# Performance work log

Hardware: AMD Instinct MI355X
Metric: run time of the kernel (lower is better)

The kernel has to match this reference:

```python
import jax, jax.numpy as jnp
import numpy as np
import math

HEADS = 4
DK = 64            # dim // heads
TEMP = 1.0
LMAX = 2048        # max segment length (for padded ragged attention)


def setup_inputs() -> dict:
    key = jax.random.key(0)
    ks = jax.random.split(key, 6)
    T, H, B = 1024, 256, 16
    # ragged lengths alternating 2048/1024 -> N = 24576
    lengths = np.tile(np.array([2048, 1024], dtype=np.int64), B // 2)
    N = int(lengths.sum())
    s = 1.0 / math.sqrt(H)
    return {
        "go_mat": jax.random.normal(ks[0], (T, H), jnp.float32),
        "node_h": jax.random.normal(ks[1], (N, H), jnp.float32),
        "Wq": jax.random.normal(ks[2], (H, H), jnp.float32) * s,
        "Wk": jax.random.normal(ks[3], (H, H), jnp.float32) * s,
        "Wv": jax.random.normal(ks[4], (H, H), jnp.float32) * s,
        "Wproj": jax.random.normal(ks[5], (H, H), jnp.float32) * s,
        "num_nodes_per_graph": jnp.asarray(lengths),
    }


def reference(go_mat, node_h, Wq, Wk, Wv, Wproj, num_nodes_per_graph):
    lengths = num_nodes_per_graph
    B = lengths.shape[0]
    N, H = node_h.shape
    T = go_mat.shape[0]

    # segment bookkeeping: graph id and within-graph offset for each node
    cum = jnp.cumsum(lengths)                       # [B]
    starts = cum - lengths                          # [B]
    g = jnp.searchsorted(cum, jnp.arange(N), side="right")  # [N] graph id
    off = jnp.arange(N) - starts[g]                 # [N] position within graph

    # projections (torch Linear: x @ W.T)
    Q = (go_mat @ Wq.T).reshape(T, HEADS, DK).transpose(1, 0, 2)   # [h,T,dk]
    K = node_h @ Wk.T                                              # [N,H]
    V = node_h @ Wv.T

    # scatter packed nodes into padded [B, Lmax, H]
    Kp = jnp.zeros((B, LMAX, H), K.dtype).at[g, off].set(K)
    Vp = jnp.zeros((B, LMAX, H), V.dtype).at[g, off].set(V)
    Kp = Kp.reshape(B, LMAX, HEADS, DK).transpose(0, 2, 1, 3)      # [B,h,L,dk]
    Vp = Vp.reshape(B, LMAX, HEADS, DK).transpose(0, 2, 1, 3)

    scores = jnp.einsum("htd,bhld->bhtl", Q, Kp) / (math.sqrt(DK) * TEMP)
    valid = jnp.arange(LMAX)[None, :] < lengths[:, None]           # [B,L]
    scores = jnp.where(valid[:, None, None, :], scores, jnp.float32(-1e30))
    attn = jax.nn.softmax(scores, axis=-1)                         # [B,h,T,L]

    ctx = jnp.einsum("bhtl,bhld->bhtd", attn, Vp)                  # [B,h,T,dk]
    ctx = ctx.transpose(0, 2, 1, 3).reshape(B, T, H)               # [B,T,H]
    return ctx @ Wproj.T
```

## Files before the change

kernel.cpp:

```cpp
#include <hip/hip_runtime.h>
#include <math.h>

#define HEADS 4
#define DK 64
#define HD 256

typedef __attribute__((ext_vector_type(8))) __bf16 bf16x8;
typedef __attribute__((ext_vector_type(4))) float floatx4;

__device__ __forceinline__ ushort f2bf(float f) {
  union { float f; unsigned u; } x; x.f = f;
  return (ushort)((x.u + 0x7FFF + ((x.u >> 16) & 1)) >> 16);
}

#if __has_builtin(__builtin_amdgcn_exp2f)
#define EXP2(x) __builtin_amdgcn_exp2f(x)
#else
#define EXP2(x) exp2f(x)
#endif

__device__ __forceinline__ unsigned pack_bf2(float lo, float hi) {
  union { float f; unsigned u; } a, b;
  a.f = lo; b.f = hi;
  return __builtin_amdgcn_perm(b.u + 0x8000u, a.u + 0x8000u, 0x07060302u);
}

#define GLDS(g, l) __builtin_amdgcn_global_load_lds(                      \
    (const __attribute__((address_space(1))) unsigned*)(g),               \
    (__attribute__((address_space(3))) unsigned*)(l), 16, 0, 0)

__global__ __launch_bounds__(256) void cvt_fused(
    const float* __restrict__ go, const float* __restrict__ nh,
    const float* __restrict__ w0, const float* __restrict__ w1,
    const float* __restrict__ w2, const float* __restrict__ w3,
    ushort* __restrict__ gobf, ushort* __restrict__ nodebf,
    ushort* __restrict__ wbf, int T, int N) {
  const int idx = blockIdx.x * 256 + threadIdx.x;
  const int row = idx >> 5, gr = idx & 31;
  if (row >= T + N + 4 * 256) return;
  const float* x; ushort* y; int r = row;
  if (row < T) { x = go; y = gobf; }
  else if (row < T + N) { x = nh; y = nodebf; r = row - T; }
  else {
    const int wr = row - T - N, wi = wr >> 8;
    r = wr & 255;
    x = (wi == 0) ? w0 : (wi == 1) ? w1 : (wi == 2) ? w2 : w3;
    y = wbf + (size_t)wi * HD * HD;
  }
  const int chunk = gr >> 3, g = gr & 7;
  const float* src = x + (size_t)r * 256 + gr * 8;
  float4 a = *(const float4*)src;
  float4 bq = *(const float4*)(src + 4);
  ushort* dst = y + (size_t)r * 256 + chunk * 64 + (g ^ (r & 7)) * 8;
  ushort4 o0 = {f2bf(a.x), f2bf(a.y), f2bf(a.z), f2bf(a.w)};
  ushort4 o1 = {f2bf(bq.x), f2bf(bq.y), f2bf(bq.z), f2bf(bq.w)};
  *(ushort4*)dst = o0;
  *(ushort4*)(dst + 4) = o1;
}

__device__ __forceinline__ void gemm_tile(const ushort* __restrict__ A,
                                          const ushort* __restrict__ W,
                                          ushort* __restrict__ C, int m0,
                                          int n0, int mode, int ldc,
                                          ushort* As, ushort* Ws, int lane,
                                          int w, int quad, int l15) {
  const int wm = w & 1, wn = w >> 1;
  floatx4 acc[4][2];
#pragma unroll
  for (int mt = 0; mt < 4; ++mt)
#pragma unroll
    for (int nt = 0; nt < 2; ++nt) acc[mt][nt] = (floatx4){0.f, 0.f, 0.f, 0.f};

  for (int k0 = 0; k0 < 256; k0 += 64) {
    __syncthreads();
#pragma unroll
    for (int t = 0; t < 4; ++t)
      GLDS(A + (size_t)(m0 + w * 32 + t * 8 + (lane >> 3)) * 256 + k0 + (lane & 7) * 8,
           &As[(w * 32 + t * 8) * 64]);
#pragma unroll
    for (int t = 0; t < 2; ++t)
      GLDS(W + (size_t)(n0 + w * 16 + t * 8 + (lane >> 3)) * 256 + k0 + (lane & 7) * 8,
           &Ws[(w * 16 + t * 8) * 64]);
    __syncthreads();

    bf16x8 af[4][2], bfr[2][2];
#pragma unroll
    for (int kk = 0; kk < 2; ++kk) {
      const int pg = ((kk * 4 + quad) ^ (l15 & 7)) * 8;
#pragma unroll
      for (int mt = 0; mt < 4; ++mt)
        af[mt][kk] = *(const bf16x8*)&As[(wm * 64 + mt * 16 + l15) * 64 + pg];
#pragma unroll
      for (int nt = 0; nt < 2; ++nt)
        bfr[nt][kk] = *(const bf16x8*)&Ws[(wn * 32 + nt * 16 + l15) * 64 + pg];
    }
#pragma unroll
    for (int kk = 0; kk < 2; ++kk)
#pragma unroll
      for (int mt = 0; mt < 4; ++mt)
#pragma unroll
        for (int nt = 0; nt < 2; ++nt)
          acc[mt][nt] = __builtin_amdgcn_mfma_f32_16x16x32_bf16(
              af[mt][kk], bfr[nt][kk], acc[mt][nt], 0, 0, 0);
  }

#pragma unroll
  for (int mt = 0; mt < 4; ++mt)
#pragma unroll
    for (int nt = 0; nt < 2; ++nt) {
      const int col = n0 + wn * 32 + nt * 16 + l15;
      if (mode == 2) {
        const int d = col & 63;
        const int g = mt * 2 + (quad >> 1);
        const int node = m0 + wm * 64 + (g ^ (d & 7)) * 8 + (quad & 1) * 4;
        ushort4 o = {f2bf(acc[mt][nt][0]), f2bf(acc[mt][nt][1]),
                     f2bf(acc[mt][nt][2]), f2bf(acc[mt][nt][3])};
        *(ushort4*)&C[(size_t)col * ldc + node] = o;
      } else {
#pragma unroll
        for (int r = 0; r < 4; ++r) {
          const int row = m0 + wm * 64 + mt * 16 + quad * 4 + r;
          if (mode == 3) {
            ((float*)C)[(size_t)row * 256 + col] = acc[mt][nt][r];
          } else {
            int cc = col;
            if (mode == 1)
              cc = (col & ~63) | (((((col >> 3) & 7) ^ (row & 7))) << 3) | (col & 7);
            C[(size_t)row * 256 + cc] = f2bf(acc[mt][nt][r]);
          }
        }
      }
    }
}

__global__ __launch_bounds__(256) void qkv_gemm(const ushort* __restrict__ gobf,
                                                const ushort* __restrict__ nodebf,
                                                const ushort* __restrict__ wbf,
                                                ushort* __restrict__ Qbf,
                                                ushort* __restrict__ Kgb,
                                                ushort* __restrict__ Vtb,
                                                int T, int N) {
  __shared__ __align__(16) ushort As[128 * 64];
  __shared__ __align__(16) ushort Ws[64 * 64];
  const int tid = threadIdx.x, lane = tid & 63, w = tid >> 6;
  const int quad = lane >> 4, l15 = lane & 15;
  const int QX = T >> 7, KB = N >> 7;
  const int NT = QX + 2 * KB;
  const int jx = blockIdx.x % NT;
  const int n0 = (blockIdx.x / NT) * 64;
  if (jx < QX)
    gemm_tile(gobf, wbf, Qbf, jx * 128, n0, 0, 0, As, Ws, lane, w, quad, l15);
  else if (jx < QX + KB)
    gemm_tile(nodebf, wbf + (size_t)HD * HD, Kgb, (jx - QX) * 128, n0, 1, 0,
              As, Ws, lane, w, quad, l15);
  else
    gemm_tile(nodebf, wbf + (size_t)2 * HD * HD, Vtb, (jx - QX - KB) * 128, n0,
              2, N, As, Ws, lane, w, quad, l15);
}

__global__ __launch_bounds__(256, 3) void attn_split(
    const ushort* __restrict__ Qb, const ushort* __restrict__ Kg,
    const ushort* __restrict__ Vt, const int* __restrict__ lens,
    float* __restrict__ Opart, float* __restrict__ Lpart,
    int T, int N, int B) {
  __shared__ __align__(16) ushort Ks[2][64 * 64];
  __shared__ __align__(16) ushort Vs[2][64 * 64];
  __shared__ __align__(16) ushort Ps[4 * 32 * 72];

  const int tid = threadIdx.x, lane = tid & 63, wave = tid >> 6;
  const int quad = lane >> 4, l15 = lane & 15;
  const int QX = T >> 7;
  const int nspl = N >> 10;
  const int grpc = HEADS * nspl;
  const int qx = blockIdx.x / grpc;
  const int rem = blockIdx.x - qx * grpc;
  const int h = rem / nspl;
  const int zid = rem - h * nspl;

  int z = zid, b, start = 0, len = 0, off = -1;
  for (b = 0; b < B; ++b) {
    len = lens[b];
    const int s = (len + 1023) >> 10;
    if (z < s) { off = z << 10; break; }
    z -= s; start += len;
  }
  if (off < 0) return;
  const int kcnt = min(1024, len - off);
  const int kbeg = start + off;

  const int q0 = qx * 128 + wave * 32;
  bf16x8 qb[2][2];
#pragma unroll
  for (int qt = 0; qt < 2; ++qt)
#pragma unroll
    for (int kk = 0; kk < 2; ++kk)
      qb[qt][kk] = *(const bf16x8*)(Qb + (size_t)(q0 + qt * 16 + l15) * 256 +
                                    h * 64 + kk * 32 + quad * 8);

  floatx4 o[2][4];
#pragma unroll
  for (int qt = 0; qt < 2; ++qt)
#pragma unroll
    for (int nt = 0; nt < 4; ++nt) o[qt][nt] = (floatx4){0.f, 0.f, 0.f, 0.f};
  float lsum[2] = {0.f, 0.f};

  const float sc = 0.18033688011112042f;
  ushort* pw = &Ps[wave * 32 * 72];
  const int srow = lane >> 3;
  const int scol = (lane & 7) * 8;

  GLDS(Kg + (size_t)(kbeg + wave * 8 + srow) * 256 + h * 64 + scol,
       &Ks[0][(wave * 8) * 64]);
  GLDS(Kg + (size_t)(kbeg + wave * 8 + 32 + srow) * 256 + h * 64 + scol,
       &Ks[0][(wave * 8 + 32) * 64]);
  GLDS(Vt + (size_t)(h * 64 + wave * 8 + srow) * (size_t)N + kbeg + scol,
       &Vs[0][(wave * 8) * 64]);
  GLDS(Vt + (size_t)(h * 64 + wave * 8 + 32 + srow) * (size_t)N + kbeg + scol,
       &Vs[0][(wave * 8 + 32) * 64]);

  int buf = 0;
  for (int j0 = 0; j0 < kcnt; j0 += 64, buf ^= 1) {
    __syncthreads();
    const int jn = j0 + 64;
    if (jn < kcnt) {
      GLDS(Kg + (size_t)(kbeg + jn + wave * 8 + srow) * 256 + h * 64 + scol,
           &Ks[buf ^ 1][(wave * 8) * 64]);
      GLDS(Kg + (size_t)(kbeg + jn + wave * 8 + 32 + srow) * 256 + h * 64 + scol,
           &Ks[buf ^ 1][(wave * 8 + 32) * 64]);
      GLDS(Vt + (size_t)(h * 64 + wave * 8 + srow) * (size_t)N + kbeg + jn + scol,
           &Vs[buf ^ 1][(wave * 8) * 64]);
      GLDS(Vt + (size_t)(h * 64 + wave * 8 + 32 + srow) * (size_t)N + kbeg + jn + scol,
           &Vs[buf ^ 1][(wave * 8 + 32) * 64]);
    }

    floatx4 st[4][2];
#pragma unroll
    for (int t = 0; t < 4; ++t)
#pragma unroll
      for (int qt = 0; qt < 2; ++qt) st[t][qt] = (floatx4){0.f, 0.f, 0.f, 0.f};
#pragma unroll
    for (int kk = 0; kk < 2; ++kk) {
#pragma unroll
      for (int t = 0; t < 4; ++t) {
        bf16x8 kf = *(const bf16x8*)&Ks[buf][(t * 16 + l15) * 64 +
                                            ((kk * 4 + quad) ^ (l15 & 7)) * 8];
        st[t][0] = __builtin_amdgcn_mfma_f32_16x16x32_bf16(kf, qb[0][kk], st[t][0], 0, 0, 0);
        st[t][1] = __builtin_amdgcn_mfma_f32_16x16x32_bf16(kf, qb[1][kk], st[t][1], 0, 0, 0);
      }
    }

    if (jn <= kcnt) {
#pragma unroll
      for (int t = 0; t < 4; ++t)
#pragma unroll
        for (int qt = 0; qt < 2; ++qt) {
          float p[4];
#pragma unroll
          for (int r = 0; r < 4; ++r) p[r] = EXP2(fmaf(st[t][qt][r], sc, -32.0f));
          lsum[qt] += (p[0] + p[1]) + (p[2] + p[3]);
          uint2 pk = {pack_bf2(p[0], p[1]), pack_bf2(p[2], p[3])};
          *(uint2*)&pw[(qt * 16 + l15) * 72 + t * 16 + quad * 4] = pk;
        }
    } else {
#pragma unroll
      for (int t = 0; t < 4; ++t)
#pragma unroll
        for (int qt = 0; qt < 2; ++qt) {
          float p[4];
#pragma unroll
          for (int r = 0; r < 4; ++r) {
            const bool v = (j0 + t * 16 + quad * 4 + r) < kcnt;
            p[r] = v ? EXP2(fmaf(st[t][qt][r], sc, -32.0f)) : 0.0f;
          }
          lsum[qt] += (p[0] + p[1]) + (p[2] + p[3]);
          uint2 pk = {pack_bf2(p[0], p[1]), pack_bf2(p[2], p[3])};
          *(uint2*)&pw[(qt * 16 + l15) * 72 + t * 16 + quad * 4] = pk;
        }
    }

#pragma unroll
    for (int ks = 0; ks < 2; ++ks) {
      bf16x8 pa0 = *(const bf16x8*)&pw[l15 * 72 + ks * 32 + quad * 8];
      bf16x8 pa1 = *(const bf16x8*)&pw[(16 + l15) * 72 + ks * 32 + quad * 8];
#pragma unroll
      for (int nt = 0; nt < 4; ++nt) {
        bf16x8 vf = *(const bf16x8*)&Vs[buf][(nt * 16 + l15) * 64 +
                                            ((ks * 4 + quad) ^ (l15 & 7)) * 8];
        o[0][nt] = __builtin_amdgcn_mfma_f32_16x16x32_bf16(pa0, vf, o[0][nt], 0, 0, 0);
        o[1][nt] = __builtin_amdgcn_mfma_f32_16x16x32_bf16(pa1, vf, o[1][nt], 0, 0, 0);
      }
    }
  }

  const int part = (zid * HEADS + h) * QX + qx;
  float* op = Opart + (size_t)part * 8192;
#pragma unroll
  for (int qt = 0; qt < 2; ++qt) {
#pragma unroll
    for (int nt = 0; nt < 4; ++nt)
#pragma unroll
      for (int r = 0; r < 4; ++r)
        op[(wave * 32 + qt * 16 + quad * 4 + r) * 64 + nt * 16 + l15] = o[qt][nt][r];
    float lt = lsum[qt];
    lt += __shfl_xor(lt, 16);
    lt += __shfl_xor(lt, 32);
    if (lane < 16)
      Lpart[(size_t)part * 128 + wave * 32 + qt * 16 + lane] = lt;
  }
}

__global__ __launch_bounds__(256) void combine(const float* __restrict__ Opart,
                                               const float* __restrict__ Lpart,
                                               const int* __restrict__ lens,
                                               ushort* __restrict__ ctxb, int T) {
  const int t = threadIdx.x;
  const int row = blockIdx.x * 64 + (t >> 2);
  const int h = t & 3;
  const int b = row / T;
  const int tq = row - b * T;
  const int qx = tq >> 7, qr = tq & 127;
  const int QX = T >> 7;
  int z0 = 0;
  for (int i = 0; i < b; ++i) z0 += (lens[i] + 1023) >> 10;
  const int ns = (lens[b] + 1023) >> 10;

  float l = 0.f;
  float4 acc[16];
#pragma unroll
  for (int g = 0; g < 16; ++g) acc[g] = make_float4(0.f, 0.f, 0.f, 0.f);
  for (int s = 0; s < ns; ++s) {
    const size_t part = (size_t)((z0 + s) * HEADS + h) * QX + qx;
    l += Lpart[part * 128 + qr];
    const float4* src = (const float4*)(Opart + part * 8192 + (size_t)qr * 64);
#pragma unroll
    for (int g = 0; g < 16; ++g) {
      float4 v = src[g];
      acc[g].x += v.x; acc[g].y += v.y; acc[g].z += v.z; acc[g].w += v.w;
    }
  }
  const float inv = 1.0f / l;
  ushort* dst = ctxb + (size_t)row * 256 + h * 64;
#pragma unroll
  for (int gg = 0; gg < 8; ++gg) {
    const float4 a = acc[gg * 2], c = acc[gg * 2 + 1];
    const int phys = gg ^ (row & 7);
    ushort4 o0 = {f2bf(a.x * inv), f2bf(a.y * inv), f2bf(a.z * inv), f2bf(a.w * inv)};
    ushort4 o1 = {f2bf(c.x * inv), f2bf(c.y * inv), f2bf(c.z * inv), f2bf(c.w * inv)};
    *(ushort4*)&dst[phys * 8] = o0;
    *(ushort4*)&dst[phys * 8 + 4] = o1;
  }
}

__global__ __launch_bounds__(256) void proj_gemm(const ushort* __restrict__ ctxb,
                                                 const ushort* __restrict__ wbf,
                                                 float* __restrict__ outp) {
  __shared__ __align__(16) ushort As[128 * 64];
  __shared__ __align__(16) ushort Ws[64 * 64];
  const int tid = threadIdx.x, lane = tid & 63, w = tid >> 6;
  const int quad = lane >> 4, l15 = lane & 15;
  gemm_tile(ctxb, wbf + (size_t)3 * HD * HD, (ushort*)outp, blockIdx.x * 128,
            blockIdx.y * 64, 3, 0, As, Ws, lane, w, quad, l15);
}

extern "C" void kernel_launch(void* const* d_in, const int* in_sizes, int n_in,
                              void* d_out, int out_size, void* d_ws, size_t ws_size,
                              hipStream_t stream) {
  const float* go     = (const float*)d_in[0];
  const float* node_h = (const float*)d_in[1];
  const float* Wq     = (const float*)d_in[2];
  const float* Wk     = (const float*)d_in[3];
  const float* Wv     = (const float*)d_in[4];
  const float* Wproj  = (const float*)d_in[5];
  const int*   lens   = (const int*)d_in[6];

  const int T = in_sizes[0] / HD;
  const int N = in_sizes[1] / HD;
  const int B = in_sizes[6];
  const int NSPL = N >> 10;
  const int QX = T >> 7;
  const int KB = N >> 7;

  char* p = (char*)d_ws;
  ushort* Kgb  = (ushort*)p;  p += (size_t)N * HD * 2;
  ushort* Vtb  = (ushort*)p;  p += (size_t)N * HD * 2;
  ushort* Qbf  = (ushort*)p;  p += (size_t)T * HD * 2;
  ushort* gobf = (ushort*)p;  p += (size_t)T * HD * 2;
  ushort* ctxb = (ushort*)p;  p += (size_t)B * T * HD * 2;
  ushort* wbf  = (ushort*)p;  p += (size_t)4 * HD * HD * 2;
  ushort* nodebf = (ushort*)p;
  float* Opart = (float*)p;   p += (size_t)NSPL * HEADS * QX * 8192 * 4;
  float* Lpart = (float*)p;   p += (size_t)NSPL * HEADS * QX * 128 * 4;

  cvt_fused<<<((T + N + 1024) * 32 + 255) / 256, 256, 0, stream>>>(
      go, node_h, Wq, Wk, Wv, Wproj, gobf, nodebf, wbf, T, N);

  qkv_gemm<<<(QX + 2 * KB) * 4, 256, 0, stream>>>(gobf, nodebf, wbf, Qbf, Kgb,
                                                  Vtb, T, N);

  attn_split<<<QX * HEADS * NSPL, 256, 0, stream>>>(Qbf, Kgb, Vtb, lens,
                                                    Opart, Lpart, T, N, B);

  combine<<<(B * T) / 64, 256, 0, stream>>>(Opart, Lpart, lens, ctxb, T);

  proj_gemm<<<dim3((B * T) / 128, 4), 256, 0, stream>>>(ctxb, wbf, (float*)d_out);
}
```

Measured before the change: 159.9 us.

## Halve attention key tile and split size, raise occupancy, adapt V swizzle

The attention kernel now processes 32-key tiles instead of 64, which shrinks the shared-memory footprint and allows launch bounds of 6 blocks per CU instead of 3. The key split per block drops from 1024 to 512 when workspace allows, which doubles the grid for better load balance. The V-transpose swizzle in the QKV GEMM is changed to match the narrower 32-column V tile. In exchange there are more loop iterations with barriers per key, and the combine kernel has to read twice as many partial outputs.

```diff
diff --git a/kernel.cpp b/kernel.cpp
--- a/kernel.cpp
+++ b/kernel.cpp
@@ -112,7 +112,8 @@
       if (mode == 2) {
         const int d = col & 63;
         const int g = mt * 2 + (quad >> 1);
-        const int node = m0 + wm * 64 + (g ^ (d & 7)) * 8 + (quad & 1) * 4;
+        const int gph = (g & 4) | ((g ^ (d & 3)) & 3);
+        const int node = m0 + wm * 64 + gph * 8 + (quad & 1) * 4;
         ushort4 o = {f2bf(acc[mt][nt][0]), f2bf(acc[mt][nt][1]),
                      f2bf(acc[mt][nt][2]), f2bf(acc[mt][nt][3])};
         *(ushort4*)&C[(size_t)col * ldc + node] = o;
@@ -158,34 +159,34 @@
               2, N, As, Ws, lane, w, quad, l15);
 }
 
-__global__ __launch_bounds__(256, 3) void attn_split(
+__global__ __launch_bounds__(256, 6) void attn_split(
     const ushort* __restrict__ Qb, const ushort* __restrict__ Kg,
     const ushort* __restrict__ Vt, const int* __restrict__ lens,
     float* __restrict__ Opart, float* __restrict__ Lpart,
-    int T, int N, int B) {
-  __shared__ __align__(16) ushort Ks[2][64 * 64];
-  __shared__ __align__(16) ushort Vs[2][64 * 64];
-  __shared__ __align__(16) ushort Ps[4 * 32 * 72];
+    int T, int N, int B, int nspl, int sh) {
+  __shared__ __align__(16) ushort Ks[2][32 * 64];
+  __shared__ __align__(16) ushort Vs[2][64 * 32];
+  __shared__ __align__(16) ushort Ps[4 * 32 * 40];
 
   const int tid = threadIdx.x, lane = tid & 63, wave = tid >> 6;
   const int quad = lane >> 4, l15 = lane & 15;
   const int QX = T >> 7;
-  const int nspl = N >> 10;
   const int grpc = HEADS * nspl;
   const int qx = blockIdx.x / grpc;
   const int rem = blockIdx.x - qx * grpc;
   const int h = rem / nspl;
   const int zid = rem - h * nspl;
 
+  const int SPL = 1 << sh;
   int z = zid, b, start = 0, len = 0, off = -1;
   for (b = 0; b < B; ++b) {
     len = lens[b];
-    const int s = (len + 1023) >> 10;
-    if (z < s) { off = z << 10; break; }
+    const int s = (len + SPL - 1) >> sh;
+    if (z < s) { off = z << sh; break; }
     z -= s; start += len;
   }
   if (off < 0) return;
-  const int kcnt = min(1024, len - off);
+  const int kcnt = min(SPL, len - off);
   const int kbeg = start + off;
 
   const int q0 = qx * 128 + wave * 32;
@@ -205,43 +206,37 @@
   float lsum[2] = {0.f, 0.f};
 
   const float sc = 0.18033688011112042f;
-  ushort* pw = &Ps[wave * 32 * 72];
+  ushort* pw = &Ps[wave * 32 * 40];
   const int srow = lane >> 3;
   const int scol = (lane & 7) * 8;
+  const int vrow = lane >> 2;
+  const int vcol = (lane & 3) * 8;
 
   GLDS(Kg + (size_t)(kbeg + wave * 8 + srow) * 256 + h * 64 + scol,
        &Ks[0][(wave * 8) * 64]);
-  GLDS(Kg + (size_t)(kbeg + wave * 8 + 32 + srow) * 256 + h * 64 + scol,
-       &Ks[0][(wave * 8 + 32) * 64]);
-  GLDS(Vt + (size_t)(h * 64 + wave * 8 + srow) * (size_t)N + kbeg + scol,
-       &Vs[0][(wave * 8) * 64]);
-  GLDS(Vt + (size_t)(h * 64 + wave * 8 + 32 + srow) * (size_t)N + kbeg + scol,
-       &Vs[0][(wave * 8 + 32) * 64]);
+  GLDS(Vt + (size_t)(h * 64 + wave * 16 + vrow) * (size_t)N + kbeg + vcol,
+       &Vs[0][(wave * 16) * 32]);
 
   int buf = 0;
-  for (int j0 = 0; j0 < kcnt; j0 += 64, buf ^= 1) {
+  for (int j0 = 0; j0 < kcnt; j0 += 32, buf ^= 1) {
     __syncthreads();
-    const int jn = j0 + 64;
+    const int jn = j0 + 32;
     if (jn < kcnt) {
       GLDS(Kg + (size_t)(kbeg + jn + wave * 8 + srow) * 256 + h * 64 + scol,
            &Ks[buf ^ 1][(wave * 8) * 64]);
-      GLDS(Kg + (size_t)(kbeg + jn + wave * 8 + 32 + srow) * 256 + h * 64 + scol,
-           &Ks[buf ^ 1][(wave * 8 + 32) * 64]);
-      GLDS(Vt + (size_t)(h * 64 + wave * 8 + srow) * (size_t)N + kbeg + jn + scol,
-           &Vs[buf ^ 1][(wave * 8) * 64]);
-      GLDS(Vt + (size_t)(h * 64 + wave * 8 + 32 + srow) * (size_t)N + kbeg + jn + scol,
-           &Vs[buf ^ 1][(wave * 8 + 32) * 64]);
-    }
-
-    floatx4 st[4][2];
-#pragma unroll
-    for (int t = 0; t < 4; ++t)
+      GLDS(Vt + (size_t)(h * 64 + wave * 16 + vrow) * (size_t)N + kbeg + jn + vcol,
+           &Vs[buf ^ 1][(wave * 16) * 32]);
+    }
+
+    floatx4 st[2][2];
+#pragma unroll
+    for (int t = 0; t < 2; ++t)
 #pragma unroll
       for (int qt = 0; qt < 2; ++qt) st[t][qt] = (floatx4){0.f, 0.f, 0.f, 0.f};
 #pragma unroll
     for (int kk = 0; kk < 2; ++kk) {
 #pragma unroll
-      for (int t = 0; t < 4; ++t) {
+      for (int t = 0; t < 2; ++t) {
         bf16x8 kf = *(const bf16x8*)&Ks[buf][(t * 16 + l15) * 64 +
                                             ((kk * 4 + quad) ^ (l15 & 7)) * 8];
         st[t][0] = __builtin_amdgcn_mfma_f32_16x16x32_bf16(kf, qb[0][kk], st[t][0], 0, 0, 0);
@@ -251,7 +246,7 @@
 
     if (jn <= kcnt) {
 #pragma unroll
-      for (int t = 0; t < 4; ++t)
+      for (int t = 0; t < 2; ++t)
 #pragma unroll
         for (int qt = 0; qt < 2; ++qt) {
           float p[4];
@@ -259,11 +254,11 @@
           for (int r = 0; r < 4; ++r) p[r] = EXP2(fmaf(st[t][qt][r], sc, -32.0f));
           lsum[qt] += (p[0] + p[1]) + (p[2] + p[3]);
           uint2 pk = {pack_bf2(p[0], p[1]), pack_bf2(p[2], p[3])};
-          *(uint2*)&pw[(qt * 16 + l15) * 72 + t * 16 + quad * 4] = pk;
+          *(uint2*)&pw[(qt * 16 + l15) * 40 + t * 16 + quad * 4] = pk;
         }
     } else {
 #pragma unroll
-      for (int t = 0; t < 4; ++t)
+      for (int t = 0; t < 2; ++t)
 #pragma unroll
         for (int qt = 0; qt < 2; ++qt) {
           float p[4];
@@ -274,21 +269,18 @@
           }
           lsum[qt] += (p[0] + p[1]) + (p[2] + p[3]);
           uint2 pk = {pack_bf2(p[0], p[1]), pack_bf2(p[2], p[3])};
-          *(uint2*)&pw[(qt * 16 + l15) * 72 + t * 16 + quad * 4] = pk;
+          *(uint2*)&pw[(qt * 16 + l15) * 40 + t * 16 + quad * 4] = pk;
         }
     }
 
-#pragma unroll
-    for (int ks = 0; ks < 2; ++ks) {
-      bf16x8 pa0 = *(const bf16x8*)&pw[l15 * 72 + ks * 32 + quad * 8];
-      bf16x8 pa1 = *(const bf16x8*)&pw[(16 + l15) * 72 + ks * 32 + quad * 8];
-#pragma unroll
-      for (int nt = 0; nt < 4; ++nt) {
-        bf16x8 vf = *(const bf16x8*)&Vs[buf][(nt * 16 + l15) * 64 +
-                                            ((ks * 4 + quad) ^ (l15 & 7)) * 8];
-        o[0][nt] = __builtin_amdgcn_mfma_f32_16x16x32_bf16(pa0, vf, o[0][nt], 0, 0, 0);
-        o[1][nt] = __builtin_amdgcn_mfma_f32_16x16x32_bf16(pa1, vf, o[1][nt], 0, 0, 0);
-      }
+    bf16x8 pa0 = *(const bf16x8*)&pw[l15 * 40 + quad * 8];
+    bf16x8 pa1 = *(const bf16x8*)&pw[(16 + l15) * 40 + quad * 8];
+#pragma unroll
+    for (int nt = 0; nt < 4; ++nt) {
+      bf16x8 vf = *(const bf16x8*)&Vs[buf][(nt * 16 + l15) * 32 +
+                                          (quad ^ (l15 & 3)) * 8];
+      o[0][nt] = __builtin_amdgcn_mfma_f32_16x16x32_bf16(pa0, vf, o[0][nt], 0, 0, 0);
+      o[1][nt] = __builtin_amdgcn_mfma_f32_16x16x32_bf16(pa1, vf, o[1][nt], 0, 0, 0);
     }
   }
 
@@ -312,7 +304,8 @@
 __global__ __launch_bounds__(256) void combine(const float* __restrict__ Opart,
                                                const float* __restrict__ Lpart,
                                                const int* __restrict__ lens,
-                                               ushort* __restrict__ ctxb, int T) {
+                                               ushort* __restrict__ ctxb, int T,
+                                               int sh) {
   const int t = threadIdx.x;
   const int row = blockIdx.x * 64 + (t >> 2);
   const int h = t & 3;
@@ -320,9 +313,10 @@
   const int tq = row - b * T;
   const int qx = tq >> 7, qr = tq & 127;
   const int QX = T >> 7;
+  const int SPL = 1 << sh;
   int z0 = 0;
-  for (int i = 0; i < b; ++i) z0 += (lens[i] + 1023) >> 10;
-  const int ns = (lens[b] + 1023) >> 10;
+  for (int i = 0; i < b; ++i) z0 += (lens[i] + SPL - 1) >> sh;
+  const int ns = (lens[b] + SPL - 1) >> sh;
 
   float l = 0.f;
   float4 acc[16];
@@ -376,9 +370,19 @@
   const int T = in_sizes[0] / HD;
   const int N = in_sizes[1] / HD;
   const int B = in_sizes[6];
-  const int NSPL = N >> 10;
   const int QX = T >> 7;
   const int KB = N >> 7;
+
+  const size_t fixed = (size_t)2 * N * HD * 2 + (size_t)2 * T * HD * 2 +
+                       (size_t)B * T * HD * 2 + (size_t)4 * HD * HD * 2;
+  int sh = 9;
+  {
+    const size_t nodebf_b = (size_t)N * HD * 2;
+    size_t part_b = (size_t)(N >> 9) * HEADS * QX * (8192 + 128) * 4;
+    if (part_b < nodebf_b) part_b = nodebf_b;
+    if (fixed + part_b > ws_size) sh = 10;
+  }
+  const int NSPL = N >> sh;
 
   char* p = (char*)d_ws;
   ushort* Kgb  = (ushort*)p;  p += (size_t)N * HD * 2;
@@ -398,9 +402,10 @@
                                                   Vtb, T, N);
 
   attn_split<<<QX * HEADS * NSPL, 256, 0, stream>>>(Qbf, Kgb, Vtb, lens,
-                                                    Opart, Lpart, T, N, B);
-
-  combine<<<(B * T) / 64, 256, 0, stream>>>(Opart, Lpart, lens, ctxb, T);
+                                                    Opart, Lpart, T, N, B,
+                                                    NSPL, sh);
+
+  combine<<<(B * T) / 64, 256, 0, stream>>>(Opart, Lpart, lens, ctxb, T, sh);
 
   proj_gemm<<<dim3((B * T) / 128, 4), 256, 0, stream>>>(ctxb, wbf, (float*)d_out);
 }
```

Measured after the change: 244.5 us. 52.9% more time.

## Load K/V fragments directly from global memory instead of staging through LDS

Applied to the files above, without the earlier changes.

The attention kernel drops the double-buffered LDS staging of K and V tiles. Each wave now reads its MFMA operand fragments straight from global memory into registers. The QKV GEMM epilogue stops writing XOR-swizzled layouts for K and V and writes them plainly. This removes the block-wide barriers and the LDS traffic, but all four waves now fetch the same K/V data independently from cache, and there is no explicit prefetch overlap.

```diff
diff --git a/kernel.cpp b/kernel.cpp
--- a/kernel.cpp
+++ b/kernel.cpp
@@ -110,9 +110,7 @@
     for (int nt = 0; nt < 2; ++nt) {
       const int col = n0 + wn * 32 + nt * 16 + l15;
       if (mode == 2) {
-        const int d = col & 63;
-        const int g = mt * 2 + (quad >> 1);
-        const int node = m0 + wm * 64 + (g ^ (d & 7)) * 8 + (quad & 1) * 4;
+        const int node = m0 + wm * 64 + mt * 16 + quad * 4;
         ushort4 o = {f2bf(acc[mt][nt][0]), f2bf(acc[mt][nt][1]),
                      f2bf(acc[mt][nt][2]), f2bf(acc[mt][nt][3])};
         *(ushort4*)&C[(size_t)col * ldc + node] = o;
@@ -123,10 +121,7 @@
           if (mode == 3) {
             ((float*)C)[(size_t)row * 256 + col] = acc[mt][nt][r];
           } else {
-            int cc = col;
-            if (mode == 1)
-              cc = (col & ~63) | (((((col >> 3) & 7) ^ (row & 7))) << 3) | (col & 7);
-            C[(size_t)row * 256 + cc] = f2bf(acc[mt][nt][r]);
+            C[(size_t)row * 256 + col] = f2bf(acc[mt][nt][r]);
           }
         }
       }
@@ -151,7 +146,7 @@
   if (jx < QX)
     gemm_tile(gobf, wbf, Qbf, jx * 128, n0, 0, 0, As, Ws, lane, w, quad, l15);
   else if (jx < QX + KB)
-    gemm_tile(nodebf, wbf + (size_t)HD * HD, Kgb, (jx - QX) * 128, n0, 1, 0,
+    gemm_tile(nodebf, wbf + (size_t)HD * HD, Kgb, (jx - QX) * 128, n0, 0, 0,
               As, Ws, lane, w, quad, l15);
   else
     gemm_tile(nodebf, wbf + (size_t)2 * HD * HD, Vtb, (jx - QX - KB) * 128, n0,
@@ -163,8 +158,6 @@
     const ushort* __restrict__ Vt, const int* __restrict__ lens,
     float* __restrict__ Opart, float* __restrict__ Lpart,
     int T, int N, int B) {
-  __shared__ __align__(16) ushort Ks[2][64 * 64];
-  __shared__ __align__(16) ushort Vs[2][64 * 64];
   __shared__ __align__(16) ushort Ps[4 * 32 * 72];
 
   const int tid = threadIdx.x, lane = tid & 63, wave = tid >> 6;
@@ -206,49 +199,40 @@
 
   const float sc = 0.18033688011112042f;
   ushort* pw = &Ps[wave * 32 * 72];
-  const int srow = lane >> 3;
-  const int scol = (lane & 7) * 8;
-
-  GLDS(Kg + (size_t)(kbeg + wave * 8 + srow) * 256 + h * 64 + scol,
-       &Ks[0][(wave * 8) * 64]);
-  GLDS(Kg + (size_t)(kbeg + wave * 8 + 32 + srow) * 256 + h * 64 + scol,
-       &Ks[0][(wave * 8 + 32) * 64]);
-  GLDS(Vt + (size_t)(h * 64 + wave * 8 + srow) * (size_t)N + kbeg + scol,
-       &Vs[0][(wave * 8) * 64]);
-  GLDS(Vt + (size_t)(h * 64 + wave * 8 + 32 + srow) * (size_t)N + kbeg + scol,
-       &Vs[0][(wave * 8 + 32) * 64]);
-
-  int buf = 0;
-  for (int j0 = 0; j0 < kcnt; j0 += 64, buf ^= 1) {
-    __syncthreads();
+
+  const ushort* kbase = Kg + (size_t)(kbeg + l15) * 256 + h * 64 + quad * 8;
+  const ushort* vbase = Vt + (size_t)(h * 64 + l15) * (size_t)N + kbeg + quad * 8;
+
+  for (int j0 = 0; j0 < kcnt; j0 += 64) {
+    bf16x8 kf[4][2];
+#pragma unroll
+    for (int t = 0; t < 4; ++t)
+#pragma unroll
+      for (int kk = 0; kk < 2; ++kk)
+        kf[t][kk] = *(const bf16x8*)(kbase + (size_t)(j0 + t * 16) * 256 + kk * 32);
+
+    floatx4 st[4][2];
+#pragma unroll
+    for (int t = 0; t < 4; ++t)
+#pragma unroll
+      for (int qt = 0; qt < 2; ++qt) st[t][qt] = (floatx4){0.f, 0.f, 0.f, 0.f};
+#pragma unroll
+    for (int kk = 0; kk < 2; ++kk)
+#pragma unroll
+      for (int t = 0; t < 4; ++t) {
+        st[t][0] = __builtin_amdgcn_mfma_f32_16x16x32_bf16(kf[t][kk], qb[0][kk], st[t][0], 0, 0, 0);
+        st[t][1] = __builtin_amdgcn_mfma_f32_16x16x32_bf16(kf[t][kk], qb[1][kk], st[t][1], 0, 0, 0);
+      }
+
+    bf16x8 vf[2][4];
+#pragma unroll
+    for (int ks = 0; ks < 2; ++ks)
+#pragma unroll
+      for (int nt = 0; nt < 4; ++nt)
+        vf[ks][nt] = *(const bf16x8*)(vbase + (size_t)(nt * 16) * (size_t)N +
+                                      j0 + ks * 32);
+
     const int jn = j0 + 64;
-    if (jn < kcnt) {
-      GLDS(Kg + (size_t)(kbeg + jn + wave * 8 + srow) * 256 + h * 64 + scol,
-           &Ks[buf ^ 1][(wave * 8) * 64]);
-      GLDS(Kg + (size_t)(kbeg + jn + wave * 8 + 32 + srow) * 256 + h * 64 + scol,
-           &Ks[buf ^ 1][(wave * 8 + 32) * 64]);
-      GLDS(Vt + (size_t)(h * 64 + wave * 8 + srow) * (size_t)N + kbeg + jn + scol,
-           &Vs[buf ^ 1][(wave * 8) * 64]);
-      GLDS(Vt + (size_t)(h * 64 + wave * 8 + 32 + srow) * (size_t)N + kbeg + jn + scol,
-           &Vs[buf ^ 1][(wave * 8 + 32) * 64]);
-    }
-
-    floatx4 st[4][2];
-#pragma unroll
-    for (int t = 0; t < 4; ++t)
-#pragma unroll
-      for (int qt = 0; qt < 2; ++qt) st[t][qt] = (floatx4){0.f, 0.f, 0.f, 0.f};
-#pragma unroll
-    for (int kk = 0; kk < 2; ++kk) {
-#pragma unroll
-      for (int t = 0; t < 4; ++t) {
-        bf16x8 kf = *(const bf16x8*)&Ks[buf][(t * 16 + l15) * 64 +
-                                            ((kk * 4 + quad) ^ (l15 & 7)) * 8];
-        st[t][0] = __builtin_amdgcn_mfma_f32_16x16x32_bf16(kf, qb[0][kk], st[t][0], 0, 0, 0);
-        st[t][1] = __builtin_amdgcn_mfma_f32_16x16x32_bf16(kf, qb[1][kk], st[t][1], 0, 0, 0);
-      }
-    }
-
     if (jn <= kcnt) {
 #pragma unroll
       for (int t = 0; t < 4; ++t)
@@ -284,10 +268,8 @@
       bf16x8 pa1 = *(const bf16x8*)&pw[(16 + l15) * 72 + ks * 32 + quad * 8];
 #pragma unroll
       for (int nt = 0; nt < 4; ++nt) {
-        bf16x8 vf = *(const bf16x8*)&Vs[buf][(nt * 16 + l15) * 64 +
-                                            ((ks * 4 + quad) ^ (l15 & 7)) * 8];
-        o[0][nt] = __builtin_amdgcn_mfma_f32_16x16x32_bf16(pa0, vf, o[0][nt], 0, 0, 0);
-        o[1][nt] = __builtin_amdgcn_mfma_f32_16x16x32_bf16(pa1, vf, o[1][nt], 0, 0, 0);
+        o[0][nt] = __builtin_amdgcn_mfma_f32_16x16x32_bf16(pa0, vf[ks][nt], o[0][nt], 0, 0, 0);
+        o[1][nt] = __builtin_amdgcn_mfma_f32_16x16x32_bf16(pa1, vf[ks][nt], o[1][nt], 0, 0, 0);
       }
     }
   }
```

Result: slower. 209.4 us (+30.9%).
